# Kernel optimization log

Hardware: AMD Instinct MI355X
Metric: run time of the kernel (lower is better)

## Reference

```python
import jax, jax.numpy as jnp
import numpy as np

B, K, N, M = 32, 128, 128, 256  # batch, num_classes(==n_dim), n_dim, samples-per-matrix
EPSILON = 0.1
LAMBDA_SOFTMAX = 0.1
LEARNING_RATE = 0.01
BN_EPS = 1e-5


def setup_inputs() -> dict:
    key = jax.random.key(0)
    k1, k2, k3 = jax.random.split(key, 3)
    x = jax.random.normal(k1, (B, N, M), dtype=jnp.float32)
    A = jax.random.normal(k2, (K, N, N), dtype=jnp.float32) * 0.1
    EC_proto = jnp.einsum('kij,klj->kil', A, A)  # per-class PSD prototype covariances (K,N,N)
    EC_count = jax.random.uniform(k3, (K,), dtype=jnp.float32, minval=1.0, maxval=100.0)
    return {"x": x, "EC_proto": EC_proto, "EC_count": EC_count}


def reference(x, EC_proto, EC_count):
    n = x.shape[1]
    dtype = x.dtype
    # BatchNorm1d(num_classes, affine=False, track_running_stats=False): batch stats over (N, L)
    mean = x.mean(axis=(0, 2), keepdims=True)
    var = x.var(axis=(0, 2), keepdims=True)  # biased variance, as torch uses for normalization
    x = (x - mean) / jnp.sqrt(var + BN_EPS)

    eye = jnp.eye(n, dtype=dtype)
    total = EC_count.sum()
    has_counts = total > 1e-6

    # E branch: global expansion operator
    e_alpha = jnp.where(has_counts, n / (EPSILON * EPSILON * total), jnp.zeros((), dtype))
    e = e_alpha * jnp.linalg.inv(e_alpha * EC_proto.sum(0) + eye)  # (N,N)
    e_x_z = jnp.einsum('ij,bjm->bim', e, x)  # (B,N,M)

    # C branch: per-class compression operators
    bool_depth = (EC_count != 0).astype(dtype)  # (K,)
    count_fix = EC_count + (1.0 - bool_depth)
    c_alpha = (n / (count_fix * EPSILON * EPSILON) * bool_depth)[:, None, None]  # (K,1,1)
    c = c_alpha * jnp.linalg.inv(c_alpha * EC_proto + eye[None])  # (K,N,N)
    c_x_z = jnp.einsum('kij,bjm->bkim', c, x)  # (B,K,N,M)

    # Frobenius norm per (b,k), rescaled to sum to 10 over classes
    norm = jnp.sqrt((c_x_z * c_x_z).sum(axis=(2, 3)))  # (B,K)
    norm = 10.0 * norm / norm.sum(axis=1, keepdims=True)

    pi = jax.nn.softmax(-LAMBDA_SOFTMAX * norm, axis=1) * bool_depth  # (B,K)
    gama = jnp.where(has_counts, EC_count / total, jnp.zeros_like(EC_count))  # (K,)

    z_d = e_x_z - jnp.einsum('k,bkim,bk->bim', gama, c_x_z, pi)  # (B,N,M)
    return x + LEARNING_RATE * z_d
```

## Files before the change

kernel.cpp:

```cpp
#include <hip/hip_runtime.h>
#include <math.h>

#define Bb 32
#define Kk 128
#define Nn 128
#define Mm 256
#define EPS2 0.01f
#define LAMBDA_S 0.1f
#define LR 0.01f
#define BN_EPS_C 1e-5f

#define SWZ(c) (((c) & 14) | (((c) & 1) << 4) | (((c) >> 4) & 1))

__device__ __forceinline__ float readlane_f(float v, int lane) {
  return __int_as_float(__builtin_amdgcn_readlane(__float_as_int(v), lane));
}

__global__ void kA_bn_psum(const float* __restrict__ x, const float* __restrict__ P,
                           float* __restrict__ xn, float* __restrict__ Psum) {
  int t = threadIdx.x;
  if (blockIdx.x < 128) {
    int n = blockIdx.x;
    float v[32];
    float s = 0.f, s2 = 0.f;
    #pragma unroll
    for (int b = 0; b < Bb; ++b) {
      v[b] = x[(size_t)b * (Nn * Mm) + n * Mm + t];
      s += v[b];
      s2 += v[b] * v[b];
    }
    #pragma unroll
    for (int o = 32; o > 0; o >>= 1) {
      s += __shfl_down(s, o, 64);
      s2 += __shfl_down(s2, o, 64);
    }
    __shared__ float rs[4], rs2[4];
    if ((t & 63) == 0) { rs[t >> 6] = s; rs2[t >> 6] = s2; }
    __syncthreads();
    float S = rs[0] + rs[1] + rs[2] + rs[3];
    float S2 = rs2[0] + rs2[1] + rs2[2] + rs2[3];
    float mean = S * (1.0f / (Bb * Mm));
    float var = S2 * (1.0f / (Bb * Mm)) - mean * mean;
    float rstd = 1.0f / sqrtf(var + BN_EPS_C);
    #pragma unroll
    for (int b = 0; b < Bb; ++b)
      xn[(size_t)b * (Nn * Mm) + n * Mm + t] = (v[b] - mean) * rstd;
  } else {
    int e = (blockIdx.x - 128) * 256 + t;
    float s = 0.f;
    #pragma unroll 8
    for (int k = 0; k < Kk; ++k) s += P[(size_t)k * 16384 + e];
    Psum[e] = s;
  }
}

__global__ __launch_bounds__(512, 1) void k3S(
    const float* __restrict__ P, const float* __restrict__ Psum,
    const float* __restrict__ cnt, float* __restrict__ C,
    const float* __restrict__ xn, float* __restrict__ S) {
  __shared__ __align__(16) float LB[8448];
  int bx = blockIdx.x;
  int t = threadIdx.x;

  if (bx < 129) {
    float* Mt = LB;
    float* Rb = LB + 2112;
    float* redc = LB + 4160;
    int mat = bx;
    int tx = t & 15;
    int wy = t >> 4;

    float cv = cnt[t & 127];
    float sr = cv;
    #pragma unroll
    for (int o = 32; o > 0; o >>= 1) sr += __shfl_down(sr, o, 64);
    if ((t & 63) == 0) redc[t >> 6] = sr;
    __syncthreads();
    float total = redc[0] + redc[1];
    bool has = total > 1e-6f;
    float av;
    if (mat < 128) {
      float c = cnt[mat];
      float bk = (c != 0.0f) ? 1.0f : 0.0f;
      float cfix = c + (1.0f - bk);
      av = (float)Nn / (cfix * EPS2) * bk;
    } else {
      av = has ? ((float)Nn / (EPS2 * total)) : 0.0f;
    }
    const float* src = (mat < 128) ? (P + (size_t)mat * 16384) : Psum;

    float a[4][8];
    #pragma unroll
    for (int i = 0; i < 4; ++i) {
      int row = wy * 4 + i;
      float4 p0 = *(const float4*)&src[row * 128 + tx * 8];
      float4 p1 = *(const float4*)&src[row * 128 + tx * 8 + 4];
      a[i][0] = av * p0.x; a[i][1] = av * p0.y; a[i][2] = av * p0.z; a[i][3] = av * p0.w;
      a[i][4] = av * p1.x; a[i][5] = av * p1.y; a[i][6] = av * p1.z; a[i][7] = av * p1.w;
      if (tx == (wy >> 1)) a[i][(wy & 1) * 4 + i] += 1.0f;
    }

    for (int kb = 0; kb < 8; ++kb) {
      int k0 = kb * 16;
      if ((wy >> 2) == kb) {
        int d = wy & 3;
        #pragma unroll
        for (int i = 0; i < 4; ++i) {
          *(float4*)&Rb[(d * 4 + i) * 128 + SWZ(2 * tx) * 4] =
              make_float4(a[i][0], a[i][1], a[i][2], a[i][3]);
          *(float4*)&Rb[(d * 4 + i) * 128 + SWZ(2 * tx + 1) * 4] =
              make_float4(a[i][4], a[i][5], a[i][6], a[i][7]);
        }
      }
      if ((tx >> 1) == kb) {
        int dh = tx & 1;
        #pragma unroll
        for (int i = 0; i < 4; ++i)
          #pragma unroll
          for (int j = 0; j < 8; ++j)
            Mt[(dh * 8 + j) * 132 + wy * 4 + i] = a[i][j];
      }
      __syncthreads();

      if (t < 64) {
        int l = t;
        float m[2][16];
        #pragma unroll
        for (int d = 0; d < 2; ++d)
          #pragma unroll
          for (int j = 0; j < 16; ++j)
            m[d][j] = Mt[j * 132 + 2 * l + d];
        #pragma unroll
        for (int q = 0; q < 16; ++q) {
          int lq = (k0 + q) >> 1;
          float pr[16];
          #pragma unroll
          for (int j = 0; j < 16; ++j) pr[j] = readlane_f(m[q & 1][j], lq);
          float piv = pr[q];
          float r0 = __builtin_amdgcn_rcpf(piv);
          float pinv = r0 * (2.0f - piv * r0);
          #pragma unroll
          for (int d = 0; d < 2; ++d) {
            float f = m[d][q];
            bool isp = (2 * l + d == k0 + q);
            float g = isp ? (1.0f - pinv) : f * pinv;
            #pragma unroll
            for (int j = 0; j < 16; ++j) m[d][j] = fmaf(-g, pr[j], m[d][j]);
            m[d][q] = isp ? pinv : -g;
          }
        }
        #pragma unroll
        for (int d = 0; d < 2; ++d)
          #pragma unroll
          for (int j = 0; j < 16; ++j)
            Mt[j * 132 + 2 * l + d] = m[d][j];
      }
      __syncthreads();

      if ((wy >> 2) == kb) {
        #pragma unroll
        for (int i = 0; i < 4; ++i)
          #pragma unroll
          for (int j = 0; j < 8; ++j) a[i][j] = 0.0f;
      }
      #pragma unroll
      for (int q = 0; q < 16; ++q) {
        float4 m0 = *(const float4*)&Mt[q * 132 + wy * 4];
        float4 r0 = *(const float4*)&Rb[q * 128 + SWZ(2 * tx) * 4];
        float4 r1 = *(const float4*)&Rb[q * 128 + SWZ(2 * tx + 1) * 4];
        float mq[4] = {m0.x, m0.y, m0.z, m0.w};
        float rq[8] = {r0.x, r0.y, r0.z, r0.w, r1.x, r1.y, r1.z, r1.w};
        #pragma unroll
        for (int i = 0; i < 4; ++i)
          #pragma unroll
          for (int j = 0; j < 8; ++j)
            a[i][j] = fmaf(mq[i], rq[j], a[i][j]);
      }
      if ((tx >> 1) == kb) {
        int dh = tx & 1;
        #pragma unroll
        for (int j = 0; j < 8; ++j) {
          float4 v0 = *(const float4*)&Mt[(dh * 8 + j) * 132 + wy * 4];
          a[0][j] = v0.x; a[1][j] = v0.y; a[2][j] = v0.z; a[3][j] = v0.w;
        }
      }
      __syncthreads();
    }

    float* dst = C + (size_t)mat * 16384;
    #pragma unroll
    for (int i = 0; i < 4; ++i) {
      int row = wy * 4 + i;
      float4 v0 = make_float4(av * a[i][0], av * a[i][1], av * a[i][2], av * a[i][3]);
      float4 v1 = make_float4(av * a[i][4], av * a[i][5], av * a[i][6], av * a[i][7]);
      *(float4*)&dst[row * 128 + tx * 8] = v0;
      *(float4*)&dst[row * 128 + tx * 8 + 4] = v1;
    }
  } else {
    int bxx = bx - 129;
    int b = bxx >> 1;
    int jbase = (bxx & 1) * 64;
    float* X = LB;
    int tx = t & 15, wy = t >> 4;
    float acc[4][4] = {};
    for (int mc = 0; mc < Mm; mc += 64) {
      __syncthreads();
      #pragma unroll
      for (int c = 0; c < 16; ++c) {
        int e = c * 512 + t;
        int i = e >> 6, mm = e & 63;
        X[i * 65 + mm] = xn[(size_t)b * (Nn * Mm) + i * Mm + mc + mm];
      }
      __syncthreads();
      for (int mm = 0; mm < 64; ++mm) {
        float ai[4], bj[4];
        #pragma unroll
        for (int q = 0; q < 4; ++q) ai[q] = X[(wy * 4 + q) * 65 + mm];
        #pragma unroll
        for (int q = 0; q < 4; ++q) bj[q] = X[(jbase + tx * 4 + q) * 65 + mm];
        #pragma unroll
        for (int qi = 0; qi < 4; ++qi)
          #pragma unroll
          for (int qj = 0; qj < 4; ++qj)
            acc[qi][qj] = fmaf(ai[qi], bj[qj], acc[qi][qj]);
      }
    }
    float* dst = S + (size_t)b * 16384;
    #pragma unroll
    for (int qi = 0; qi < 4; ++qi) {
      float4 v = make_float4(acc[qi][0], acc[qi][1], acc[qi][2], acc[qi][3]);
      *(float4*)&dst[(wy * 4 + qi) * 128 + jbase + tx * 4] = v;
    }
  }
}

__global__ __launch_bounds__(256, 1) void kGN(const float* __restrict__ C,
                                              const float* __restrict__ S,
                                              float* __restrict__ norm2h) {
  __shared__ __align__(16) float LB[128 * 128];
  __shared__ float redb[4][32];
  int k = blockIdx.x >> 2, qh = blockIdx.x & 3;
  int t = threadIdx.x;
  const float* src = C + (size_t)k * 16384;
  for (int c = 0; c < 64; ++c) LB[c * 256 + t] = src[c * 256 + t];
  __syncthreads();
  int tx = t & 15, ty = t >> 4;
  int i0 = ty * 8, j0 = qh * 32 + tx * 2;
  float acc[8][2] = {};
  #pragma unroll 2
  for (int l = 0; l < 128; ++l) {
    float ai[8];
    *(float4*)&ai[0] = *(const float4*)&LB[l * 128 + i0];
    *(float4*)&ai[4] = *(const float4*)&LB[l * 128 + i0 + 4];
    float2 bj = *(const float2*)&LB[l * 128 + j0];
    #pragma unroll
    for (int qi = 0; qi < 8; ++qi) {
      acc[qi][0] = fmaf(ai[qi], bj.x, acc[qi][0]);
      acc[qi][1] = fmaf(ai[qi], bj.y, acc[qi][1]);
    }
  }
  __syncthreads();
  #pragma unroll
  for (int qi = 0; qi < 8; ++qi)
    *(float2*)&LB[(i0 + qi) * 32 + tx * 2] = make_float2(acc[qi][0], acc[qi][1]);
  __syncthreads();
  float nacc[32];
  #pragma unroll
  for (int b = 0; b < 32; ++b) nacc[b] = 0.0f;
  #pragma unroll
  for (int q = 0; q < 4; ++q) {
    int el = (q * 256 + t) * 4;
    float4 g = *(const float4*)&LB[el];
    int i = el >> 5, jl = el & 31;
    const float* sb = S + i * 128 + qh * 32 + jl;
    #pragma unroll
    for (int b = 0; b < 32; ++b) {
      float4 sv = *(const float4*)&sb[(size_t)b * 16384];
      nacc[b] = fmaf(g.x, sv.x, nacc[b]);
      nacc[b] = fmaf(g.y, sv.y, nacc[b]);
      nacc[b] = fmaf(g.z, sv.z, nacc[b]);
      nacc[b] = fmaf(g.w, sv.w, nacc[b]);
    }
  }
  #pragma unroll
  for (int b = 0; b < 32; ++b) {
    float v = nacc[b];
    #pragma unroll
    for (int o = 32; o > 0; o >>= 1) v += __shfl_down(v, o, 64);
    nacc[b] = v;
  }
  if ((t & 63) == 0) {
    int w = t >> 6;
    #pragma unroll
    for (int b = 0; b < 32; ++b) redb[w][b] = nacc[b];
  }
  __syncthreads();
  if (t < 32)
    norm2h[(size_t)k * 128 + qh * 32 + t] =
        redb[0][t] + redb[1][t] + redb[2][t] + redb[3][t];
}

__global__ __launch_bounds__(256, 1) void k8f(const float* __restrict__ C,
                                              const float* __restrict__ E,
                                              const float* __restrict__ norm2h,
                                              const float* __restrict__ cnt,
                                              float* __restrict__ F) {
  int t = threadIdx.x;
  int e = blockIdx.x * 256 + t;
  int b0 = blockIdx.y * 8;
  __shared__ float wTl[128][8];
  __shared__ float redT[2];
  __shared__ float redN[2][8];
  __shared__ float redE[2][8];

  float nb[8];
  float cv = 0.f;
  if (t < 128) {
    int k = t;
    cv = cnt[k];
    #pragma unroll
    for (int j = 0; j < 8; ++j) {
      const float* nh = norm2h + (size_t)k * 128 + b0 + j;
      float n2 = nh[0] + nh[32] + nh[64] + nh[96];
      nb[j] = sqrtf(fmaxf(n2, 0.0f));
    }
    float tt = cv;
    float sn[8];
    #pragma unroll
    for (int j = 0; j < 8; ++j) sn[j] = nb[j];
    #pragma unroll
    for (int o = 32; o > 0; o >>= 1) {
      tt += __shfl_down(tt, o, 64);
      #pragma unroll
      for (int j = 0; j < 8; ++j) sn[j] += __shfl_down(sn[j], o, 64);
    }
    if ((t & 63) == 0) {
      redT[t >> 6] = tt;
      #pragma unroll
      for (int j = 0; j < 8; ++j) redN[t >> 6][j] = sn[j];
    }
  }
  __syncthreads();
  float exj[8];
  if (t < 128) {
    #pragma unroll
    for (int j = 0; j < 8; ++j) {
      float sumn = fmaxf(redN[0][j] + redN[1][j], 1e-30f);
      float nr = 10.0f * nb[j] / sumn;
      exj[j] = expf(-LAMBDA_S * nr);
    }
    float se[8];
    #pragma unroll
    for (int j = 0; j < 8; ++j) se[j] = exj[j];
    #pragma unroll
    for (int o = 32; o > 0; o >>= 1) {
      #pragma unroll
      for (int j = 0; j < 8; ++j) se[j] += __shfl_down(se[j], o, 64);
    }
    if ((t & 63) == 0) {
      #pragma unroll
      for (int j = 0; j < 8; ++j) redE[t >> 6][j] = se[j];
    }
  }
  __syncthreads();
  if (t < 128) {
    float total = redT[0] + redT[1];
    float bk = (cv != 0.0f) ? 1.0f : 0.0f;
    float gama = (total > 1e-6f) ? (cv / total) : 0.0f;
    #pragma unroll
    for (int j = 0; j < 8; ++j) {
      float sume = redE[0][j] + redE[1][j];
      float pi = (exj[j] / sume) * bk;
      wTl[t][j] = gama * pi;
    }
  }
  __syncthreads();

  float acc[8];
  float ev = E[e];
  #pragma unroll
  for (int b = 0; b < 8; ++b) acc[b] = ev;
  #pragma unroll 4
  for (int k = 0; k < 128; ++k) {
    float cval = C[(size_t)k * 16384 + e];
    #pragma unroll
    for (int b = 0; b < 8; ++b) acc[b] = fmaf(-wTl[k][b], cval, acc[b]);
  }
  #pragma unroll
  for (int b = 0; b < 8; ++b) F[(size_t)(b0 + b) * 16384 + e] = acc[b];
}

__global__ __launch_bounds__(512, 1) void k9_k(const float* __restrict__ F,
                                               const float* __restrict__ xn,
                                               float* __restrict__ out) {
  int bx = blockIdx.x;
  int b = bx >> 3, y = bx & 7;
  int mq = y >> 1, ih = y & 1;
  __shared__ __align__(16) float Ft[64 * 68];
  __shared__ __align__(16) float Xt[64 * 68];
  int t = threadIdx.x;
  int tx = t & 15, ty = t >> 4;
  float acc[2][4] = {};
  for (int jc = 0; jc < 128; jc += 64) {
    __syncthreads();
    #pragma unroll
    for (int q = 0; q < 2; ++q) {
      int e = q * 512 + t;
      int i = e >> 4, j4 = e & 15;
      *(float4*)&Ft[i * 68 + j4 * 4] =
          *(const float4*)&F[(size_t)b * 16384 + (ih * 64 + i) * 128 + jc + j4 * 4];
    }
    #pragma unroll
    for (int q = 0; q < 2; ++q) {
      int e = q * 512 + t;
      int jj = e >> 4, m4 = e & 15;
      *(float4*)&Xt[jj * 68 + m4 * 4] =
          *(const float4*)&xn[(size_t)b * (Nn * Mm) + (jc + jj) * Mm + mq * 64 + m4 * 4];
    }
    __syncthreads();
    for (int j4 = 0; j4 < 16; ++j4) {
      float4 fi[2], xm[4];
      #pragma unroll
      for (int r = 0; r < 2; ++r)
        fi[r] = *(const float4*)&Ft[(ty * 2 + r) * 68 + j4 * 4];
      #pragma unroll
      for (int r = 0; r < 4; ++r)
        xm[r] = *(const float4*)&Xt[(j4 * 4 + r) * 68 + tx * 4];
      #pragma unroll
      for (int qi = 0; qi < 2; ++qi) {
        #pragma unroll
        for (int qm = 0; qm < 4; ++qm) {
          float xv = ((const float*)&xm[0])[qm];
          acc[qi][qm] = fmaf(fi[qi].x, xv, acc[qi][qm]);
          xv = ((const float*)&xm[1])[qm];
          acc[qi][qm] = fmaf(fi[qi].y, xv, acc[qi][qm]);
          xv = ((const float*)&xm[2])[qm];
          acc[qi][qm] = fmaf(fi[qi].z, xv, acc[qi][qm]);
          xv = ((const float*)&xm[3])[qm];
          acc[qi][qm] = fmaf(fi[qi].w, xv, acc[qi][qm]);
        }
      }
    }
  }
  int i0 = ih * 64 + ty * 2, m0 = mq * 64 + tx * 4;
  #pragma unroll
  for (int qi = 0; qi < 2; ++qi) {
    float4 xv = *(const float4*)&xn[(size_t)b * (Nn * Mm) + (i0 + qi) * Mm + m0];
    float4 o;
    o.x = fmaf(LR, acc[qi][0], xv.x);
    o.y = fmaf(LR, acc[qi][1], xv.y);
    o.z = fmaf(LR, acc[qi][2], xv.z);
    o.w = fmaf(LR, acc[qi][3], xv.w);
    *(float4*)&out[(size_t)b * (Nn * Mm) + (i0 + qi) * Mm + m0] = o;
  }
}

extern "C" void kernel_launch(void* const* d_in, const int* in_sizes, int n_in,
                              void* d_out, int out_size, void* d_ws, size_t ws_size,
                              hipStream_t stream) {
  const float* x = (const float*)d_in[0];
  const float* P = (const float*)d_in[1];
  const float* cnt = (const float*)d_in[2];
  float* out = (float*)d_out;

  float* ws = (float*)d_ws;
  float* xn = ws;
  float* C = xn + 1048576;
  float* S = C + 2113536;
  float* norm2h = S + 524288;
  float* F = norm2h + 16384;
  float* Psum = F + 524288;
  size_t need_bytes = (size_t)((Psum + 16384) - ws) * sizeof(float);
  if (ws_size < need_bytes) return;

  hipLaunchKernelGGL(kA_bn_psum, dim3(192), dim3(256), 0, stream, x, P, xn, Psum);
  hipLaunchKernelGGL(k3S, dim3(193), dim3(512), 0, stream, P, Psum, cnt, C, xn, S);
  hipLaunchKernelGGL(kGN, dim3(512), dim3(256), 0, stream, C, S, norm2h);
  hipLaunchKernelGGL(k8f, dim3(64, 4), dim3(256), 0, stream, C,
                     C + (size_t)128 * 16384, norm2h, cnt, F);
  hipLaunchKernelGGL(k9_k, dim3(256), dim3(512), 0, stream, F, xn, out);
}
```

Before: 159.0 us.

## Compute Gram matrices on raw x and fold BatchNorm in algebraically

```diff
diff --git a/kernel.cpp b/kernel.cpp
--- a/kernel.cpp
+++ b/kernel.cpp
@@ -16,48 +16,20 @@
   return __int_as_float(__builtin_amdgcn_readlane(__float_as_int(v), lane));
 }
 
-__global__ void kA_bn_psum(const float* __restrict__ x, const float* __restrict__ P,
-                           float* __restrict__ xn, float* __restrict__ Psum) {
-  int t = threadIdx.x;
-  if (blockIdx.x < 128) {
-    int n = blockIdx.x;
-    float v[32];
-    float s = 0.f, s2 = 0.f;
-    #pragma unroll
-    for (int b = 0; b < Bb; ++b) {
-      v[b] = x[(size_t)b * (Nn * Mm) + n * Mm + t];
-      s += v[b];
-      s2 += v[b] * v[b];
-    }
-    #pragma unroll
-    for (int o = 32; o > 0; o >>= 1) {
-      s += __shfl_down(s, o, 64);
-      s2 += __shfl_down(s2, o, 64);
-    }
-    __shared__ float rs[4], rs2[4];
-    if ((t & 63) == 0) { rs[t >> 6] = s; rs2[t >> 6] = s2; }
-    __syncthreads();
-    float S = rs[0] + rs[1] + rs[2] + rs[3];
-    float S2 = rs2[0] + rs2[1] + rs2[2] + rs2[3];
-    float mean = S * (1.0f / (Bb * Mm));
-    float var = S2 * (1.0f / (Bb * Mm)) - mean * mean;
-    float rstd = 1.0f / sqrtf(var + BN_EPS_C);
-    #pragma unroll
-    for (int b = 0; b < Bb; ++b)
-      xn[(size_t)b * (Nn * Mm) + n * Mm + t] = (v[b] - mean) * rstd;
-  } else {
-    int e = (blockIdx.x - 128) * 256 + t;
-    float s = 0.f;
-    #pragma unroll 8
-    for (int k = 0; k < Kk; ++k) s += P[(size_t)k * 16384 + e];
-    Psum[e] = s;
-  }
-}
-
-__global__ __launch_bounds__(512, 1) void k3S(
+__global__ void kPre(const float* __restrict__ P, float* __restrict__ Psum) {
+  int e = blockIdx.x * 256 + threadIdx.x;
+  float s = 0.f;
+  #pragma unroll 8
+  for (int k = 0; k < Kk; ++k) s += P[(size_t)k * 16384 + e];
+  Psum[e] = s;
+}
+
+__global__ __launch_bounds__(512, 1) void kBig(
     const float* __restrict__ P, const float* __restrict__ Psum,
     const float* __restrict__ cnt, float* __restrict__ C,
-    const float* __restrict__ xn, float* __restrict__ S) {
+    const float* __restrict__ x, float* __restrict__ R,
+    float* __restrict__ rbuf, float* __restrict__ meanB,
+    float* __restrict__ rstdB, float* __restrict__ xn) {
   __shared__ __align__(16) float LB[8448];
   int bx = blockIdx.x;
   int t = threadIdx.x;
@@ -196,22 +168,27 @@
       *(float4*)&dst[row * 128 + tx * 8] = v0;
       *(float4*)&dst[row * 128 + tx * 8 + 4] = v1;
     }
-  } else {
+  } else if (bx < 193) {
     int bxx = bx - 129;
     int b = bxx >> 1;
     int jbase = (bxx & 1) * 64;
     float* X = LB;
     int tx = t & 15, wy = t >> 4;
     float acc[4][4] = {};
+    float rsum = 0.f;
     for (int mc = 0; mc < Mm; mc += 64) {
       __syncthreads();
       #pragma unroll
       for (int c = 0; c < 16; ++c) {
         int e = c * 512 + t;
         int i = e >> 6, mm = e & 63;
-        X[i * 65 + mm] = xn[(size_t)b * (Nn * Mm) + i * Mm + mc + mm];
+        X[i * 65 + mm] = x[(size_t)b * (Nn * Mm) + i * Mm + mc + mm];
       }
       __syncthreads();
+      if (t < 128) {
+        #pragma unroll
+        for (int mm = 0; mm < 64; ++mm) rsum += X[t * 65 + mm];
+      }
       for (int mm = 0; mm < 64; ++mm) {
         float ai[4], bj[4];
         #pragma unroll
@@ -225,22 +202,55 @@
             acc[qi][qj] = fmaf(ai[qi], bj[qj], acc[qi][qj]);
       }
     }
-    float* dst = S + (size_t)b * 16384;
+    float* dst = R + (size_t)b * 16384;
     #pragma unroll
     for (int qi = 0; qi < 4; ++qi) {
       float4 v = make_float4(acc[qi][0], acc[qi][1], acc[qi][2], acc[qi][3]);
       *(float4*)&dst[(wy * 4 + qi) * 128 + jbase + tx * 4] = v;
     }
+    if (jbase == 0 && t < 128) rbuf[b * 128 + t] = rsum;
+  } else {
+    int n = bx - 193;
+    int m = t & 255, bh = t >> 8;
+    float v[16];
+    float s = 0.f, s2 = 0.f;
+    #pragma unroll
+    for (int q = 0; q < 16; ++q) {
+      v[q] = x[(size_t)(bh * 16 + q) * (Nn * Mm) + n * Mm + m];
+      s += v[q]; s2 += v[q] * v[q];
+    }
+    #pragma unroll
+    for (int o = 32; o > 0; o >>= 1) {
+      s += __shfl_down(s, o, 64);
+      s2 += __shfl_down(s2, o, 64);
+    }
+    if ((t & 63) == 0) { LB[t >> 6] = s; LB[16 + (t >> 6)] = s2; }
+    __syncthreads();
+    float S = 0.f, S2 = 0.f;
+    #pragma unroll
+    for (int w = 0; w < 8; ++w) { S += LB[w]; S2 += LB[16 + w]; }
+    float mean = S * (1.0f / (Bb * Mm));
+    float var = S2 * (1.0f / (Bb * Mm)) - mean * mean;
+    float rstd = 1.0f / sqrtf(var + BN_EPS_C);
+    if (t == 0) { meanB[n] = mean; rstdB[n] = rstd; }
+    #pragma unroll
+    for (int q = 0; q < 16; ++q)
+      xn[(size_t)(bh * 16 + q) * (Nn * Mm) + n * Mm + m] = (v[q] - mean) * rstd;
   }
 }
 
 __global__ __launch_bounds__(256, 1) void kGN(const float* __restrict__ C,
-                                              const float* __restrict__ S,
+                                              const float* __restrict__ R,
+                                              const float* __restrict__ rbuf,
+                                              const float* __restrict__ meanB,
+                                              const float* __restrict__ rstdB,
                                               float* __restrict__ norm2h) {
   __shared__ __align__(16) float LB[128 * 128];
   __shared__ float redb[4][32];
+  __shared__ float muL[128], rsL[128], uL[128];
   int k = blockIdx.x >> 2, qh = blockIdx.x & 3;
   int t = threadIdx.x;
+  if (t < 128) { muL[t] = meanB[t]; rsL[t] = rstdB[t]; }
   const float* src = C + (size_t)k * 16384;
   for (int c = 0; c < 64; ++c) LB[c * 256 + t] = src[c * 256 + t];
   __syncthreads();
@@ -260,10 +270,21 @@
     }
   }
   __syncthreads();
-  #pragma unroll
-  for (int qi = 0; qi < 8; ++qi)
-    *(float2*)&LB[(i0 + qi) * 32 + tx * 2] = make_float2(acc[qi][0], acc[qi][1]);
-  __syncthreads();
+  float sj0 = rsL[j0], sj1 = rsL[j0 + 1];
+  #pragma unroll
+  for (int qi = 0; qi < 8; ++qi) {
+    float si = rsL[i0 + qi];
+    *(float2*)&LB[(i0 + qi) * 32 + tx * 2] =
+        make_float2(acc[qi][0] * si * sj0, acc[qi][1] * si * sj1);
+  }
+  __syncthreads();
+  if (t < 128) {
+    float u = 0.f;
+    #pragma unroll
+    for (int jl = 0; jl < 32; ++jl)
+      u = fmaf(LB[t * 32 + jl], muL[qh * 32 + jl], u);
+    uL[t] = u;
+  }
   float nacc[32];
   #pragma unroll
   for (int b = 0; b < 32; ++b) nacc[b] = 0.0f;
@@ -272,7 +293,7 @@
     int el = (q * 256 + t) * 4;
     float4 g = *(const float4*)&LB[el];
     int i = el >> 5, jl = el & 31;
-    const float* sb = S + i * 128 + qh * 32 + jl;
+    const float* sb = R + i * 128 + qh * 32 + jl;
     #pragma unroll
     for (int b = 0; b < 32; ++b) {
       float4 sv = *(const float4*)&sb[(size_t)b * 16384];
@@ -295,9 +316,13 @@
     for (int b = 0; b < 32; ++b) redb[w][b] = nacc[b];
   }
   __syncthreads();
-  if (t < 32)
+  if (t < 32) {
+    float corr = 0.f;
+    for (int i = 0; i < 128; ++i)
+      corr = fmaf(uL[i], 256.0f * muL[i] - 2.0f * rbuf[t * 128 + i], corr);
     norm2h[(size_t)k * 128 + qh * 32 + t] =
-        redb[0][t] + redb[1][t] + redb[2][t] + redb[3][t];
+        redb[0][t] + redb[1][t] + redb[2][t] + redb[3][t] + corr;
+  }
 }
 
 __global__ __launch_bounds__(256, 1) void k8f(const float* __restrict__ C,
@@ -466,16 +491,21 @@
   float* ws = (float*)d_ws;
   float* xn = ws;
   float* C = xn + 1048576;
-  float* S = C + 2113536;
-  float* norm2h = S + 524288;
+  float* R = C + 2113536;
+  float* norm2h = R + 524288;
   float* F = norm2h + 16384;
   float* Psum = F + 524288;
-  size_t need_bytes = (size_t)((Psum + 16384) - ws) * sizeof(float);
+  float* rbuf = Psum + 16384;
+  float* meanB = rbuf + 4096;
+  float* rstdB = meanB + 128;
+  size_t need_bytes = (size_t)((rstdB + 128) - ws) * sizeof(float);
   if (ws_size < need_bytes) return;
 
-  hipLaunchKernelGGL(kA_bn_psum, dim3(192), dim3(256), 0, stream, x, P, xn, Psum);
-  hipLaunchKernelGGL(k3S, dim3(193), dim3(512), 0, stream, P, Psum, cnt, C, xn, S);
-  hipLaunchKernelGGL(kGN, dim3(512), dim3(256), 0, stream, C, S, norm2h);
+  hipLaunchKernelGGL(kPre, dim3(64), dim3(256), 0, stream, P, Psum);
+  hipLaunchKernelGGL(kBig, dim3(321), dim3(512), 0, stream, P, Psum, cnt, C, x,
+                     R, rbuf, meanB, rstdB, xn);
+  hipLaunchKernelGGL(kGN, dim3(512), dim3(256), 0, stream, C, R, rbuf, meanB,
+                     rstdB, norm2h);
   hipLaunchKernelGGL(k8f, dim3(64, 4), dim3(256), 0, stream, C,
                      C + (size_t)128 * 16384, norm2h, cnt, F);
   hipLaunchKernelGGL(k9_k, dim3(256), dim3(512), 0, stream, F, xn, out);
```

Measured after the change: 162.1 us. About the same (+1.9%).
